# Kernel optimization log

Hardware: AMD Instinct MI355X
Metric: run time of the kernel (lower is better)

The kernel has to match this reference:

```python
import jax, jax.numpy as jnp
import numpy as np

SHAPES = [(100, 100), (50, 50), (25, 25), (13, 13)]
EMBED, HEADS, LEVELS, POINTS = 256, 8, 4, 4
DH = EMBED // HEADS


def setup_inputs() -> dict:
    key = jax.random.key(0)
    ks = jax.random.split(key, 12)
    bs, nq = 4, 10000
    nv = sum(h * w for h, w in SHAPES)
    s = 0.02
    return {
        'query': jax.random.normal(ks[0], (bs, nq, EMBED), jnp.float32),
        'value': jax.random.normal(ks[1], (bs, nv, EMBED), jnp.float32),
        'reference_points': jax.random.uniform(ks[2], (bs, nq, LEVELS, 2), jnp.float32),
        'spatial_shapes': jnp.array(SHAPES, jnp.int32),
        'Wv': s * jax.random.normal(ks[3], (EMBED, EMBED), jnp.float32),
        'bv': jnp.zeros((EMBED,), jnp.float32),
        'Woff': s * jax.random.normal(ks[4], (EMBED, HEADS * LEVELS * POINTS * 2), jnp.float32),
        'boff': s * jax.random.normal(ks[5], (HEADS * LEVELS * POINTS * 2,), jnp.float32),
        'Ww': s * jax.random.normal(ks[6], (EMBED, HEADS * LEVELS * POINTS), jnp.float32),
        'bw': jnp.zeros((HEADS * LEVELS * POINTS,), jnp.float32),
        'Wo': s * jax.random.normal(ks[7], (EMBED, EMBED), jnp.float32),
        'bo': jnp.zeros((EMBED,), jnp.float32),
    }


def _msda(v, loc, aw, bs, nq):
    # v: (bs, nv, heads, dh); loc: (bs, nq, heads, L, P, 2) normalized in [0,1]
    # aw: (bs, nq, heads, L, P). Bilinear grid_sample, align_corners=False, zero padding.
    out = jnp.zeros((bs, HEADS, nq, DH), v.dtype)
    start = 0
    for l, (H, W) in enumerate(SHAPES):
        vl = v[:, start:start + H * W].transpose(0, 2, 1, 3)  # (bs, heads, H*W, dh)
        start += H * W
        locl = loc[:, :, :, l]                                # (bs, nq, heads, P, 2)
        x = locl[..., 0] * W - 0.5                            # align_corners=False mapping
        y = locl[..., 1] * H - 0.5
        x0 = jnp.floor(x); y0 = jnp.floor(y)
        fx = x - x0; fy = y - y0
        x0i = x0.astype(jnp.int32); y0i = y0.astype(jnp.int32)
        sampled = jnp.zeros((bs, HEADS, nq * POINTS, DH), v.dtype)
        for dy, wy in ((0, 1.0 - fy), (1, fy)):
            for dx, wx in ((0, 1.0 - fx), (1, fx)):
                xi = x0i + dx; yi = y0i + dy
                valid = (xi >= 0) & (xi < W) & (yi >= 0) & (yi < H)
                idx = jnp.clip(yi, 0, W and H - 1) * W + jnp.clip(xi, 0, W - 1)
                idx = jnp.clip(yi, 0, H - 1) * W + jnp.clip(xi, 0, W - 1)
                idx_t = idx.transpose(0, 2, 1, 3).reshape(bs, HEADS, nq * POINTS)
                g = jnp.take_along_axis(vl, idx_t[..., None], axis=2)  # (bs,heads,nq*P,dh)
                w = jnp.where(valid, wx * wy, 0.0).transpose(0, 2, 1, 3).reshape(bs, HEADS, -1)
                sampled = sampled + g * w[..., None]
        awl = aw[:, :, :, l].transpose(0, 2, 1, 3).reshape(bs, HEADS, nq * POINTS)
        out = out + (sampled * awl[..., None]).reshape(bs, HEADS, nq, POINTS, DH).sum(3)
    return out.transpose(0, 2, 1, 3).reshape(bs, nq, EMBED)


def reference(query, value, reference_points, spatial_shapes, Wv, bv, Woff, boff, Ww, bw, Wo, bo):
    bs, nq, _ = query.shape
    v = (value @ Wv + bv).reshape(bs, -1, HEADS, DH)
    off = (query @ Woff + boff).reshape(bs, nq, HEADS, LEVELS, POINTS, 2)
    aw = jax.nn.softmax((query @ Ww + bw).reshape(bs, nq, HEADS, LEVELS * POINTS), axis=-1)
    aw = aw.reshape(bs, nq, HEADS, LEVELS, POINTS)
    normalizer = jnp.stack([spatial_shapes[:, 1], spatial_shapes[:, 0]], -1).astype(query.dtype)  # (L,2) = (W,H)
    loc = reference_points[:, :, None, :, None, :] + off / normalizer[None, None, None, :, None, :]
    out = _msda(v, loc, aw, bs, nq)
    out = out @ Wo + bo
    return out + query  # identity residual (dropout in eval mode)
```

## Files before the change

### kernel.cpp

```cpp
#include <hip/hip_runtime.h>
#include <hip/hip_fp16.h>

#define BS     4
#define NQ     10000
#define NV     13294
#define EMBED  256
#define HEADS  8
#define LEVELS 4
#define POINTS 4
#define DH     32

#define MV_PAD 53248
#define MQ_PAD 40064

typedef __attribute__((ext_vector_type(8))) _Float16 half8;
typedef __attribute__((ext_vector_type(4))) float floatx4;

static __device__ __forceinline__ unsigned short f2h(float f) {
    __half h = __float2half(f);
    return *(unsigned short*)&h;
}
static __device__ __forceinline__ float h2f(unsigned short u) {
    __half h = *(__half*)&u;
    return __half2float(h);
}
static __device__ __forceinline__ unsigned int pk_f16(float x, float y) {
    __half2 h = __floats2half2_rn(x, y);
    unsigned int u; __builtin_memcpy(&u, &h, 4); return u;
}

static __device__ __forceinline__ void gload_lds16(const unsigned short* g, unsigned short* l) {
    __builtin_amdgcn_global_load_lds(
        (const __attribute__((address_space(1))) void*)g,
        (__attribute__((address_space(3))) void*)l,
        16, 0, 0);
}

#define CONV_BLOCKS 2048

__global__ __launch_bounds__(256) void prep_convert(
    const float* __restrict__ Wv,  const float* __restrict__ Woff,
    const float* __restrict__ boff,const float* __restrict__ Ww,
    const float* __restrict__ bw,  const float* __restrict__ Wo,
    const float* __restrict__ value, const float* __restrict__ query,
    unsigned short* __restrict__ Wvt, unsigned short* __restrict__ Wcatt,
    unsigned short* __restrict__ Wot, float* __restrict__ bcat,
    unsigned short* __restrict__ v16, unsigned short* __restrict__ q16)
{
    const int n = blockIdx.x;
    const int k = threadIdx.x;
    if (n < 896) {
        if (n < 256) {
            Wvt[n * 256 + k] = f2h(Wv[k * 256 + n]);
        } else if (n < 512) {
            Wcatt[(n - 256) * 256 + k] = f2h(Woff[k * 256 + (n - 256)]);
        } else if (n < 640) {
            Wcatt[(n - 256) * 256 + k] = f2h(Ww[k * 128 + (n - 512)]);
        } else {
            Wot[(n - 640) * 256 + k] = f2h(Wo[k * 256 + (n - 640)]);
        }
        if (n == 0) {
            for (int j = k; j < 384; j += 256)
                bcat[j] = (j < 256) ? boff[j] : bw[j - 256];
        }
        return;
    }
    const long long NV8 = (long long)BS * NV * 256 / 8;
    const long long NQ8 = (long long)BS * NQ * 256 / 8;
    const long long stride = (long long)CONV_BLOCKS * 256;
    for (long long u = (long long)(n - 896) * 256 + k; u < NV8 + NQ8; u += stride) {
        const float4* s;
        unsigned short* d;
        if (u < NV8) { s = (const float4*)value + u * 2;         d = v16 + u * 8; }
        else         { s = (const float4*)query + (u - NV8) * 2; d = q16 + (u - NV8) * 8; }
        const float4 f0 = s[0], f1 = s[1];
        uint4 o;
        o.x = pk_f16(f0.x, f0.y);
        o.y = pk_f16(f0.z, f0.w);
        o.z = pk_f16(f1.x, f1.y);
        o.w = pk_f16(f1.z, f1.w);
        *(uint4*)d = o;
    }
}

template<int MODE>
static __device__ __forceinline__ void gemm_body(
    unsigned short* As, unsigned short* Bs,
    const unsigned short* __restrict__ A, int M,
    const unsigned short* __restrict__ Bt,
    const float* __restrict__ bias,
    void* __restrict__ Cv, int ldc,
    const float* __restrict__ residual,
    int mb, int nb)
{
    const int t    = threadIdx.x;
    const int w    = t >> 6;
    const int lane = t & 63;
    const int m0 = mb * 128;
    const int n0 = nb * 128;
    const int wm = (w & 1) * 64;
    const int wn = (w >> 1) * 64;
    const int lr = lane & 15;
    const int lk = (lane >> 4) * 8;

    const int srow = w * 8 + (lane >> 3);
    const int scol = ((lane & 7) ^ (lane >> 3)) * 8;
    const unsigned short* ga = A  + (size_t)(m0 + srow) * 256 + scol;
    const unsigned short* gb = Bt + (size_t)(n0 + srow) * 256 + scol;
    unsigned short* lA = As + w * 512;
    unsigned short* lB = Bs + w * 512;

    floatx4 acc[4][4] = {};

    for (int k0 = 0; k0 < 256; k0 += 64) {
        __syncthreads();
        #pragma unroll
        for (int j = 0; j < 4; ++j) {
            gload_lds16(ga + (size_t)j * 32 * 256 + k0, lA + j * 2048);
            gload_lds16(gb + (size_t)j * 32 * 256 + k0, lB + j * 2048);
        }
        __syncthreads();

        #pragma unroll
        for (int kk = 0; kk < 64; kk += 32) {
            half8 bf[4];
            #pragma unroll
            for (int nt = 0; nt < 4; ++nt) {
                const int row = wn + nt * 16 + lr;
                const int cb  = ((kk + lk) * 2) ^ ((row & 7) << 4);
                bf[nt] = *(const half8*)((const char*)Bs + row * 128 + cb);
            }
            #pragma unroll
            for (int mt = 0; mt < 4; ++mt) {
                const int row = wm + mt * 16 + lr;
                const int cb  = ((kk + lk) * 2) ^ ((row & 7) << 4);
                const half8 af = *(const half8*)((const char*)As + row * 128 + cb);
                #pragma unroll
                for (int nt = 0; nt < 4; ++nt)
                    acc[mt][nt] = __builtin_amdgcn_mfma_f32_16x16x32_f16(af, bf[nt], acc[mt][nt], 0, 0, 0);
            }
        }
    }

    const int rbase = m0 + wm + (lane >> 4) * 4;
    #pragma unroll
    for (int nt = 0; nt < 4; ++nt) {
        const int col = n0 + wn + nt * 16 + lr;
        const float bb_ = bias[col];
        #pragma unroll
        for (int mt = 0; mt < 4; ++mt) {
            #pragma unroll
            for (int r = 0; r < 4; ++r) {
                const int row = rbase + mt * 16 + r;
                if (row < M) {
                    float val = acc[mt][nt][r] + bb_;
                    if (MODE == 2) val += residual[(size_t)row * ldc + col];
                    if (MODE == 0) {
                        ((unsigned short*)Cv)[(size_t)row * ldc + col] = f2h(val);
                    } else if (MODE == 3) {
                        const int b_ = row / NV;
                        const int s_ = row - b_ * NV;
                        const int h_ = col >> 5, d_ = col & 31;
                        ((unsigned short*)Cv)[(((size_t)b_ * 8 + h_) * NV + s_) * 32 + d_] = f2h(val);
                    } else {
                        ((float*)Cv)[(size_t)row * ldc + col] = val;
                    }
                }
            }
        }
    }
}

__global__ __launch_bounds__(256) void gemm_fused12(
    const unsigned short* __restrict__ v16, const unsigned short* __restrict__ q16,
    const unsigned short* __restrict__ Wvt, const unsigned short* __restrict__ Wcatt,
    const float* __restrict__ bv, const float* __restrict__ bcat,
    unsigned short* __restrict__ vout, unsigned short* __restrict__ projout)
{
    __shared__ __align__(16) unsigned short As[128 * 64];
    __shared__ __align__(16) unsigned short Bs[128 * 64];
    const unsigned int xcd = blockIdx.x & 7u, kk = blockIdx.x >> 3;
    const unsigned int wg = (xcd < 3u ? xcd * 222u : 3u * 222u + (xcd - 3u) * 221u) + kk;
    if (wg < 832u) {
        gemm_body<3>(As, Bs, v16, BS * NV, Wvt, bv, vout, 256, nullptr,
                     (int)(wg >> 1), (int)(wg & 1));
    } else {
        const unsigned int b2 = wg - 832u;
        gemm_body<0>(As, Bs, q16, BS * NQ, Wcatt, bcat, projout, 384, nullptr,
                     (int)(b2 / 3u), (int)(b2 % 3u));
    }
}

__global__ __launch_bounds__(256) void gemm_out(
    const unsigned short* __restrict__ msda, const unsigned short* __restrict__ Wot,
    const float* __restrict__ bo, float* __restrict__ out,
    const float* __restrict__ query)
{
    __shared__ __align__(16) unsigned short As[128 * 64];
    __shared__ __align__(16) unsigned short Bs[128 * 64];
    const unsigned int xcd = blockIdx.x & 7u, kk = blockIdx.x >> 3;
    const unsigned int wg = (xcd < 2u ? xcd * 79u : 2u * 79u + (xcd - 2u) * 78u) + kk;
    gemm_body<2>(As, Bs, msda, BS * NQ, Wot, bo, out, 256, query,
                 (int)(wg >> 1), (int)(wg & 1));
}

__global__ __launch_bounds__(256) void msda_sample(
    const unsigned short* __restrict__ v,
    const unsigned short* __restrict__ proj,
    const float* __restrict__ rp,
    unsigned short* __restrict__ out)
{
    __shared__ __align__(16) unsigned int taps[4 * 2112];

    const unsigned int bid = blockIdx.x;
    const int h      = (int)(bid & 7u);
    const int b      = (int)((bid >> 3) & 3u);
    const int qchunk = (int)(bid >> 5);
    const int wave = threadIdx.x >> 6;
    const int lane = threadIdx.x & 63;
    const int qi   = lane >> 2;
    const int li   = lane & 3;
    const int q    = qchunk * 64 + wave * 16 + qi;
    const bool qok = q < NQ;
    const int rowq = b * NQ + (qok ? q : 0);
    const unsigned short* prow = proj + (size_t)rowq * 384;

    const ushort4 lg = *(const ushort4*)&prow[256 + h * 16 + li * 4];
    const float l0 = h2f(lg.x), l1 = h2f(lg.y), l2 = h2f(lg.z), l3 = h2f(lg.w);
    float mx = fmaxf(fmaxf(l0, l1), fmaxf(l2, l3));
    mx = fmaxf(mx, __shfl_xor(mx, 1));
    mx = fmaxf(mx, __shfl_xor(mx, 2));
    const float e0 = __expf(l0 - mx);
    const float e1 = __expf(l1 - mx);
    const float e2 = __expf(l2 - mx);
    const float e3 = __expf(l3 - mx);
    float ssum = (e0 + e1) + (e2 + e3);
    ssum += __shfl_xor(ssum, 1);
    ssum += __shfl_xor(ssum, 2);
    const float inv = 1.0f / ssum;
    const float ev[4] = {e0 * inv, e1 * inv, e2 * inv, e3 * inv};

    const int Wl = (li == 0) ? 100 : (li == 1) ? 50 : (li == 2) ? 25 : 13;
    const int st = (li == 0) ? 0 : (li == 1) ? 10000 : (li == 2) ? 12500 : 13125;
    const float fW = (float)Wl, fH = (float)Wl;

    const float2 rxy = *(const float2*)&rp[((size_t)rowq * 4 + li) * 2];

    const uint4 offu = *(const uint4*)&prow[h * 32 + li * 8];
    const unsigned int opk[4] = {offu.x, offu.y, offu.z, offu.w};

    unsigned int* tbase = taps + wave * 2112 + qi * 132;

    #pragma unroll
    for (int p = 0; p < 4; ++p) {
        const float ox = h2f((unsigned short)(opk[p] & 0xFFFFu));
        const float oy = h2f((unsigned short)(opk[p] >> 16));
        const float aww = ev[p];
        const float x = fmaf(rxy.x, fW, ox) - 0.5f;
        const float y = fmaf(rxy.y, fH, oy) - 0.5f;
        const float x0f = floorf(x), y0f = floorf(y);
        const float fx = x - x0f, fy = y - y0f;
        const int ix = (int)x0f, iy = (int)y0f;
        const float wxv[2] = {1.f - fx, fx};
        const float wyv[2] = {1.f - fy, fy};

        unsigned int offv[4]; float wv_[4];
        #pragma unroll
        for (int tp = 0; tp < 4; ++tp) {
            const int dy = tp >> 1, dx = tp & 1;
            const int xi = ix + dx, yi = iy + dy;
            const bool ok = (xi >= 0) && (xi < Wl) && (yi >= 0) && (yi < Wl);
            const int cx = min(max(xi, 0), Wl - 1);
            const int cy = min(max(yi, 0), Wl - 1);
            offv[tp] = (unsigned int)(st + cy * Wl + cx) * 64u;
            wv_[tp]  = ok ? wyv[dy] * wxv[dx] * aww : 0.f;
        }
        const uint4 eA = make_uint4(offv[0], offv[1], pk_f16(wv_[0], wv_[0]), pk_f16(wv_[1], wv_[1]));
        const uint4 eB = make_uint4(offv[2], offv[3], pk_f16(wv_[2], wv_[2]), pk_f16(wv_[3], wv_[3]));
        *(uint4*)&tbase[(li * 8 + p * 2) * 4]     = eA;
        *(uint4*)&tbase[(li * 8 + p * 2 + 1) * 4] = eB;
    }

    asm volatile("s_waitcnt lgkmcnt(0)" ::: "memory");

    const unsigned int lane_off = (unsigned int)li * 16u;
    const char* vbase = (const char*)v + ((size_t)b * 8 + h) * (size_t)NV * 64;
    const uint4* tp4 = (const uint4*)(taps + wave * 2112 + qi * 132);

    __half2 a0 = __floats2half2_rn(0.f, 0.f);
    __half2 a1 = a0, a2 = a0, a3 = a0;
    #pragma unroll 8
    for (int j = 0; j < 32; ++j) {
        const uint4 ee = tp4[j];
        const uint4 g0 = *(const uint4*)(vbase + (ee.x + lane_off));
        const uint4 g1 = *(const uint4*)(vbase + (ee.y + lane_off));
        __half2 w0, w1, t0, t1, t2, t3;
        __builtin_memcpy(&w0, &ee.z, 4);
        __builtin_memcpy(&w1, &ee.w, 4);
        __builtin_memcpy(&t0, &g0.x, 4);
        __builtin_memcpy(&t1, &g0.y, 4);
        __builtin_memcpy(&t2, &g0.z, 4);
        __builtin_memcpy(&t3, &g0.w, 4);
        a0 = __hfma2(t0, w0, a0);
        a1 = __hfma2(t1, w0, a1);
        a2 = __hfma2(t2, w0, a2);
        a3 = __hfma2(t3, w0, a3);
        __builtin_memcpy(&t0, &g1.x, 4);
        __builtin_memcpy(&t1, &g1.y, 4);
        __builtin_memcpy(&t2, &g1.z, 4);
        __builtin_memcpy(&t3, &g1.w, 4);
        a0 = __hfma2(t0, w1, a0);
        a1 = __hfma2(t1, w1, a1);
        a2 = __hfma2(t2, w1, a2);
        a3 = __hfma2(t3, w1, a3);
    }

    if (qok) {
        uint4 o;
        __builtin_memcpy(&o.x, &a0, 4);
        __builtin_memcpy(&o.y, &a1, 4);
        __builtin_memcpy(&o.z, &a2, 4);
        __builtin_memcpy(&o.w, &a3, 4);
        *(uint4*)&out[(size_t)rowq * 256 + h * 32 + li * 8] = o;
    }
}

extern "C" void kernel_launch(void* const* d_in, const int* in_sizes, int n_in,
                              void* d_out, int out_size, void* d_ws, size_t ws_size,
                              hipStream_t stream) {
    const float* query = (const float*)d_in[0];
    const float* value = (const float*)d_in[1];
    const float* rp    = (const float*)d_in[2];
    const float* Wv    = (const float*)d_in[4];
    const float* bv    = (const float*)d_in[5];
    const float* Woff  = (const float*)d_in[6];
    const float* boff  = (const float*)d_in[7];
    const float* Ww    = (const float*)d_in[8];
    const float* bw    = (const float*)d_in[9];
    const float* Wo    = (const float*)d_in[10];
    const float* bo    = (const float*)d_in[11];
    float* out = (float*)d_out;

    const int Mq = BS * NQ;

    char* ws = (char*)d_ws;
    const size_t SZ_MSDA = (size_t)MQ_PAD * 256 * 2;
    const size_t SZ_VIN  = (size_t)MV_PAD * 256 * 2;
    const size_t SZ_QIN  = (size_t)MQ_PAD * 256 * 2;
    const size_t SZ_VPR  = (size_t)BS * NV * 256 * 2;
    const size_t SZ_PROJ = (size_t)Mq * 384 * 2;

    unsigned short* msda  = (unsigned short*)(ws);
    unsigned short* v16   = (unsigned short*)(ws + SZ_MSDA);
    unsigned short* q16   = (unsigned short*)(ws + SZ_MSDA + SZ_VIN);
    unsigned short* v_prj = (unsigned short*)(ws + SZ_MSDA + SZ_VIN + SZ_QIN);
    unsigned short* proj  = (unsigned short*)(ws + SZ_MSDA + SZ_VIN + SZ_QIN + SZ_VPR);
    char* wp = ws + SZ_MSDA + SZ_VIN + SZ_QIN + SZ_VPR + SZ_PROJ;
    unsigned short* Wvt   = (unsigned short*)(wp);
    unsigned short* Wcatt = (unsigned short*)(wp + 256 * 256 * 2);
    unsigned short* Wot   = (unsigned short*)(wp + 256 * 256 * 2 + 384 * 256 * 2);
    float*          bcat  = (float*)(wp + 256 * 256 * 2 + 384 * 256 * 2 + 256 * 256 * 2);

    prep_convert<<<896 + CONV_BLOCKS, 256, 0, stream>>>(
        Wv, Woff, boff, Ww, bw, Wo, value, query,
        Wvt, Wcatt, Wot, bcat, v16, q16);

    gemm_fused12<<<832 + 939, 256, 0, stream>>>(
        v16, q16, Wvt, Wcatt, bv, bcat, v_prj, proj);

    msda_sample<<<157 * 32, 256, 0, stream>>>(v_prj, proj, rp, msda);

    gemm_out<<<626, 256, 0, stream>>>(msda, Wot, bo, out, query);
}
```

Baseline: 289.2 us.

## Fuse fp32-to-fp16 input conversion into GEMM loads and compact sampling taps

The separate pass that converted value and query to fp16 is removed. The projection GEMM now loads fp32 rows straight into a larger LDS tile and converts them to fp16 when it builds the MFMA fragments, which saves a full read and write of the activations through HBM. Separately, the MSDA tap table now stores two 16-bit cell indices and packed fp16 weights per entry, halving its LDS footprint and the per-iteration LDS read size. The costs are a doubled A-tile in LDS, conversion work inside the GEMM inner loop, and the assumption that cell indices fit in 16 bits (NV is 13294, so they do).

Result: no change. 290.3 us (+0.4%).

```diff
diff --git a/kernel.cpp b/kernel.cpp
--- a/kernel.cpp
+++ b/kernel.cpp
@@ -10,7 +10,6 @@
 #define POINTS 4
 #define DH     32
 
-#define MV_PAD 53248
 #define MQ_PAD 40064
 
 typedef __attribute__((ext_vector_type(8))) _Float16 half8;
@@ -29,64 +28,41 @@
     unsigned int u; __builtin_memcpy(&u, &h, 4); return u;
 }
 
-static __device__ __forceinline__ void gload_lds16(const unsigned short* g, unsigned short* l) {
+static __device__ __forceinline__ void gload_lds16(const void* g, void* l) {
     __builtin_amdgcn_global_load_lds(
         (const __attribute__((address_space(1))) void*)g,
         (__attribute__((address_space(3))) void*)l,
         16, 0, 0);
 }
 
-#define CONV_BLOCKS 2048
-
-__global__ __launch_bounds__(256) void prep_convert(
+__global__ __launch_bounds__(256) void prep_weights(
     const float* __restrict__ Wv,  const float* __restrict__ Woff,
     const float* __restrict__ boff,const float* __restrict__ Ww,
     const float* __restrict__ bw,  const float* __restrict__ Wo,
-    const float* __restrict__ value, const float* __restrict__ query,
     unsigned short* __restrict__ Wvt, unsigned short* __restrict__ Wcatt,
-    unsigned short* __restrict__ Wot, float* __restrict__ bcat,
-    unsigned short* __restrict__ v16, unsigned short* __restrict__ q16)
+    unsigned short* __restrict__ Wot, float* __restrict__ bcat)
 {
     const int n = blockIdx.x;
     const int k = threadIdx.x;
-    if (n < 896) {
-        if (n < 256) {
-            Wvt[n * 256 + k] = f2h(Wv[k * 256 + n]);
-        } else if (n < 512) {
-            Wcatt[(n - 256) * 256 + k] = f2h(Woff[k * 256 + (n - 256)]);
-        } else if (n < 640) {
-            Wcatt[(n - 256) * 256 + k] = f2h(Ww[k * 128 + (n - 512)]);
-        } else {
-            Wot[(n - 640) * 256 + k] = f2h(Wo[k * 256 + (n - 640)]);
-        }
-        if (n == 0) {
-            for (int j = k; j < 384; j += 256)
-                bcat[j] = (j < 256) ? boff[j] : bw[j - 256];
-        }
-        return;
-    }
-    const long long NV8 = (long long)BS * NV * 256 / 8;
-    const long long NQ8 = (long long)BS * NQ * 256 / 8;
-    const long long stride = (long long)CONV_BLOCKS * 256;
-    for (long long u = (long long)(n - 896) * 256 + k; u < NV8 + NQ8; u += stride) {
-        const float4* s;
-        unsigned short* d;
-        if (u < NV8) { s = (const float4*)value + u * 2;         d = v16 + u * 8; }
-        else         { s = (const float4*)query + (u - NV8) * 2; d = q16 + (u - NV8) * 8; }
-        const float4 f0 = s[0], f1 = s[1];
-        uint4 o;
-        o.x = pk_f16(f0.x, f0.y);
-        o.y = pk_f16(f0.z, f0.w);
-        o.z = pk_f16(f1.x, f1.y);
-        o.w = pk_f16(f1.z, f1.w);
-        *(uint4*)d = o;
-    }
-}
-
-template<int MODE>
+    if (n < 256) {
+        Wvt[n * 256 + k] = f2h(Wv[k * 256 + n]);
+    } else if (n < 512) {
+        Wcatt[(n - 256) * 256 + k] = f2h(Woff[k * 256 + (n - 256)]);
+    } else if (n < 640) {
+        Wcatt[(n - 256) * 256 + k] = f2h(Ww[k * 128 + (n - 512)]);
+    } else {
+        Wot[(n - 640) * 256 + k] = f2h(Wo[k * 256 + (n - 640)]);
+    }
+    if (n == 0) {
+        for (int j = k; j < 384; j += 256)
+            bcat[j] = (j < 256) ? boff[j] : bw[j - 256];
+    }
+}
+
+template<int MODE, bool AF32>
 static __device__ __forceinline__ void gemm_body(
-    unsigned short* As, unsigned short* Bs,
-    const unsigned short* __restrict__ A, int M,
+    void* AsR, unsigned short* Bs,
+    const void* __restrict__ A, int M,
     const unsigned short* __restrict__ Bt,
     const float* __restrict__ bias,
     void* __restrict__ Cv, int ldc,
@@ -103,21 +79,44 @@
     const int lr = lane & 15;
     const int lk = (lane >> 4) * 8;
 
-    const int srow = w * 8 + (lane >> 3);
-    const int scol = ((lane & 7) ^ (lane >> 3)) * 8;
-    const unsigned short* ga = A  + (size_t)(m0 + srow) * 256 + scol;
-    const unsigned short* gb = Bt + (size_t)(n0 + srow) * 256 + scol;
-    unsigned short* lA = As + w * 512;
+    const int srowB = w * 8 + (lane >> 3);
+    const int scolB = ((lane & 7) ^ (lane >> 3)) * 8;
+    const unsigned short* gb = Bt + (size_t)(n0 + srowB) * 256 + scolB;
     unsigned short* lB = Bs + w * 512;
+
+    const unsigned short* gaH = nullptr; unsigned short* lAH = nullptr;
+    const float* gaF = nullptr; char* lAF = nullptr;
+    int rowA0 = 0, scAF = 0;
+    if constexpr (AF32) {
+        rowA0 = w * 4 + (lane >> 4);
+        scAF = ((lane & 15) ^ (rowA0 & 7)) * 4;
+        gaF = (const float*)A;
+        lAF = (char*)AsR + w * 1024;
+    } else {
+        gaH = (const unsigned short*)A + (size_t)(m0 + srowB) * 256 + scolB;
+        lAH = (unsigned short*)AsR + w * 512;
+    }
 
     floatx4 acc[4][4] = {};
 
     for (int k0 = 0; k0 < 256; k0 += 64) {
         __syncthreads();
-        #pragma unroll
-        for (int j = 0; j < 4; ++j) {
-            gload_lds16(ga + (size_t)j * 32 * 256 + k0, lA + j * 2048);
-            gload_lds16(gb + (size_t)j * 32 * 256 + k0, lB + j * 2048);
+        if constexpr (AF32) {
+            #pragma unroll
+            for (int j = 0; j < 8; ++j) {
+                int r = m0 + rowA0 + j * 16;
+                r = min(r, M - 1);
+                gload_lds16(gaF + (size_t)r * 256 + k0 + scAF, lAF + j * 4096);
+            }
+            #pragma unroll
+            for (int j = 0; j < 4; ++j)
+                gload_lds16(gb + (size_t)j * 32 * 256 + k0, lB + j * 2048);
+        } else {
+            #pragma unroll
+            for (int j = 0; j < 4; ++j) {
+                gload_lds16(gaH + (size_t)j * 32 * 256 + k0, lAH + j * 2048);
+                gload_lds16(gb + (size_t)j * 32 * 256 + k0, lB + j * 2048);
+            }
         }
         __syncthreads();
 
@@ -133,8 +132,20 @@
             #pragma unroll
             for (int mt = 0; mt < 4; ++mt) {
                 const int row = wm + mt * 16 + lr;
-                const int cb  = ((kk + lk) * 2) ^ ((row & 7) << 4);
-                const half8 af = *(const half8*)((const char*)As + row * 128 + cb);
+                half8 af;
+                if constexpr (AF32) {
+                    const int base = (kk + lk) * 4;
+                    const int sw   = (row & 7) << 4;
+                    const float4 f0 = *(const float4*)((const char*)AsR + row * 256 + (base ^ sw));
+                    const float4 f1 = *(const float4*)((const char*)AsR + row * 256 + ((base + 16) ^ sw));
+                    uint4 u;
+                    u.x = pk_f16(f0.x, f0.y); u.y = pk_f16(f0.z, f0.w);
+                    u.z = pk_f16(f1.x, f1.y); u.w = pk_f16(f1.z, f1.w);
+                    __builtin_memcpy(&af, &u, 16);
+                } else {
+                    const int cb = ((kk + lk) * 2) ^ ((row & 7) << 4);
+                    af = *(const half8*)((const char*)AsR + row * 128 + cb);
+                }
                 #pragma unroll
                 for (int nt = 0; nt < 4; ++nt)
                     acc[mt][nt] = __builtin_amdgcn_mfma_f32_16x16x32_f16(af, bf[nt], acc[mt][nt], 0, 0, 0);
@@ -172,22 +183,22 @@
 }
 
 __global__ __launch_bounds__(256) void gemm_fused12(
-    const unsigned short* __restrict__ v16, const unsigned short* __restrict__ q16,
+    const float* __restrict__ value, const float* __restrict__ query,
     const unsigned short* __restrict__ Wvt, const unsigned short* __restrict__ Wcatt,
     const float* __restrict__ bv, const float* __restrict__ bcat,
     unsigned short* __restrict__ vout, unsigned short* __restrict__ projout)
 {
-    __shared__ __align__(16) unsigned short As[128 * 64];
+    __shared__ __align__(16) char As4[32768];
     __shared__ __align__(16) unsigned short Bs[128 * 64];
     const unsigned int xcd = blockIdx.x & 7u, kk = blockIdx.x >> 3;
     const unsigned int wg = (xcd < 3u ? xcd * 222u : 3u * 222u + (xcd - 3u) * 221u) + kk;
     if (wg < 832u) {
-        gemm_body<3>(As, Bs, v16, BS * NV, Wvt, bv, vout, 256, nullptr,
-                     (int)(wg >> 1), (int)(wg & 1));
+        gemm_body<3, true>(As4, Bs, value, BS * NV, Wvt, bv, vout, 256, nullptr,
+                           (int)(wg >> 1), (int)(wg & 1));
     } else {
         const unsigned int b2 = wg - 832u;
-        gemm_body<0>(As, Bs, q16, BS * NQ, Wcatt, bcat, projout, 384, nullptr,
-                     (int)(b2 / 3u), (int)(b2 % 3u));
+        gemm_body<0, true>(As4, Bs, query, BS * NQ, Wcatt, bcat, projout, 384, nullptr,
+                           (int)(b2 / 3u), (int)(b2 % 3u));
     }
 }
 
@@ -200,8 +211,8 @@
     __shared__ __align__(16) unsigned short Bs[128 * 64];
     const unsigned int xcd = blockIdx.x & 7u, kk = blockIdx.x >> 3;
     const unsigned int wg = (xcd < 2u ? xcd * 79u : 2u * 79u + (xcd - 2u) * 78u) + kk;
-    gemm_body<2>(As, Bs, msda, BS * NQ, Wot, bo, out, 256, query,
-                 (int)(wg >> 1), (int)(wg & 1));
+    gemm_body<2, false>(As, Bs, msda, BS * NQ, Wot, bo, out, 256, query,
+                        (int)(wg >> 1), (int)(wg & 1));
 }
 
 __global__ __launch_bounds__(256) void msda_sample(
@@ -210,7 +221,7 @@
     const float* __restrict__ rp,
     unsigned short* __restrict__ out)
 {
-    __shared__ __align__(16) unsigned int taps[4 * 2112];
+    __shared__ __align__(16) unsigned int taps[4 * 1088];
 
     const unsigned int bid = blockIdx.x;
     const int h      = (int)(bid & 7u);
@@ -249,7 +260,7 @@
     const uint4 offu = *(const uint4*)&prow[h * 32 + li * 8];
     const unsigned int opk[4] = {offu.x, offu.y, offu.z, offu.w};
 
-    unsigned int* tbase = taps + wave * 2112 + qi * 132;
+    unsigned int* tbase = taps + wave * 1088 + qi * 68;
 
     #pragma unroll
     for (int p = 0; p < 4; ++p) {
@@ -264,7 +275,7 @@
         const float wxv[2] = {1.f - fx, fx};
         const float wyv[2] = {1.f - fy, fy};
 
-        unsigned int offv[4]; float wv_[4];
+        unsigned int cellv[4]; float wv_[4];
         #pragma unroll
         for (int tp = 0; tp < 4; ++tp) {
             const int dy = tp >> 1, dx = tp & 1;
@@ -272,31 +283,35 @@
             const bool ok = (xi >= 0) && (xi < Wl) && (yi >= 0) && (yi < Wl);
             const int cx = min(max(xi, 0), Wl - 1);
             const int cy = min(max(yi, 0), Wl - 1);
-            offv[tp] = (unsigned int)(st + cy * Wl + cx) * 64u;
-            wv_[tp]  = ok ? wyv[dy] * wxv[dx] * aww : 0.f;
+            cellv[tp] = (unsigned int)(st + cy * Wl + cx);
+            wv_[tp]   = ok ? wyv[dy] * wxv[dx] * aww : 0.f;
         }
-        const uint4 eA = make_uint4(offv[0], offv[1], pk_f16(wv_[0], wv_[0]), pk_f16(wv_[1], wv_[1]));
-        const uint4 eB = make_uint4(offv[2], offv[3], pk_f16(wv_[2], wv_[2]), pk_f16(wv_[3], wv_[3]));
-        *(uint4*)&tbase[(li * 8 + p * 2) * 4]     = eA;
-        *(uint4*)&tbase[(li * 8 + p * 2 + 1) * 4] = eB;
+        uint4 e;
+        e.x = cellv[0] | (cellv[1] << 16);
+        e.y = pk_f16(wv_[0], wv_[1]);
+        e.z = cellv[2] | (cellv[3] << 16);
+        e.w = pk_f16(wv_[2], wv_[3]);
+        *(uint4*)&tbase[(li * 8 + p * 2) * 2] = e;
     }
 
     asm volatile("s_waitcnt lgkmcnt(0)" ::: "memory");
 
     const unsigned int lane_off = (unsigned int)li * 16u;
     const char* vbase = (const char*)v + ((size_t)b * 8 + h) * (size_t)NV * 64;
-    const uint4* tp4 = (const uint4*)(taps + wave * 2112 + qi * 132);
+    const uint2* tp2 = (const uint2*)(taps + wave * 1088 + qi * 68);
 
     __half2 a0 = __floats2half2_rn(0.f, 0.f);
     __half2 a1 = a0, a2 = a0, a3 = a0;
     #pragma unroll 8
     for (int j = 0; j < 32; ++j) {
-        const uint4 ee = tp4[j];
-        const uint4 g0 = *(const uint4*)(vbase + (ee.x + lane_off));
-        const uint4 g1 = *(const uint4*)(vbase + (ee.y + lane_off));
-        __half2 w0, w1, t0, t1, t2, t3;
-        __builtin_memcpy(&w0, &ee.z, 4);
-        __builtin_memcpy(&w1, &ee.w, 4);
+        const uint2 ee = tp2[j];
+        const uint4 g0 = *(const uint4*)(vbase + ((ee.x & 0xFFFFu) << 6) + lane_off);
+        const uint4 g1 = *(const uint4*)(vbase + ((ee.x >> 16) << 6) + lane_off);
+        __half2 wpk;
+        __builtin_memcpy(&wpk, &ee.y, 4);
+        const __half2 w0 = __low2half2(wpk);
+        const __half2 w1 = __high2half2(wpk);
+        __half2 t0, t1, t2, t3;
         __builtin_memcpy(&t0, &g0.x, 4);
         __builtin_memcpy(&t1, &g0.y, 4);
         __builtin_memcpy(&t2, &g0.z, 4);
@@ -345,28 +360,23 @@
 
     char* ws = (char*)d_ws;
     const size_t SZ_MSDA = (size_t)MQ_PAD * 256 * 2;
-    const size_t SZ_VIN  = (size_t)MV_PAD * 256 * 2;
-    const size_t SZ_QIN  = (size_t)MQ_PAD * 256 * 2;
     const size_t SZ_VPR  = (size_t)BS * NV * 256 * 2;
     const size_t SZ_PROJ = (size_t)Mq * 384 * 2;
 
     unsigned short* msda  = (unsigned short*)(ws);
-    unsigned short* v16   = (unsigned short*)(ws + SZ_MSDA);
-    unsigned short* q16   = (unsigned short*)(ws + SZ_MSDA + SZ_VIN);
-    unsigned short* v_prj = (unsigned short*)(ws + SZ_MSDA + SZ_VIN + SZ_QIN);
-    unsigned short* proj  = (unsigned short*)(ws + SZ_MSDA + SZ_VIN + SZ_QIN + SZ_VPR);
-    char* wp = ws + SZ_MSDA + SZ_VIN + SZ_QIN + SZ_VPR + SZ_PROJ;
+    unsigned short* v_prj = (unsigned short*)(ws + SZ_MSDA);
+    unsigned short* proj  = (unsigned short*)(ws + SZ_MSDA + SZ_VPR);
+    char* wp = ws + SZ_MSDA + SZ_VPR + SZ_PROJ;
     unsigned short* Wvt   = (unsigned short*)(wp);
     unsigned short* Wcatt = (unsigned short*)(wp + 256 * 256 * 2);
     unsigned short* Wot   = (unsigned short*)(wp + 256 * 256 * 2 + 384 * 256 * 2);
     float*          bcat  = (float*)(wp + 256 * 256 * 2 + 384 * 256 * 2 + 256 * 256 * 2);
 
-    prep_convert<<<896 + CONV_BLOCKS, 256, 0, stream>>>(
-        Wv, Woff, boff, Ww, bw, Wo, value, query,
-        Wvt, Wcatt, Wot, bcat, v16, q16);
+    prep_weights<<<896, 256, 0, stream>>>(
+        Wv, Woff, boff, Ww, bw, Wo, Wvt, Wcatt, Wot, bcat);
 
     gemm_fused12<<<832 + 939, 256, 0, stream>>>(
-        v16, q16, Wvt, Wcatt, bv, bcat, v_prj, proj);
+        value, query, Wvt, Wcatt, bv, bcat, v_prj, proj);
 
     msda_sample<<<157 * 32, 256, 0, stream>>>(v_prj, proj, rp, msda);
 
```
